# Kernel tuning notes

Hardware: AMD Instinct MI355X
Metric: run time of the kernel (lower is better)

## Reference

```python
import jax, jax.numpy as jnp
import numpy as np
from jax import lax

B, T, H, W, E = 64, 8, 8, 8, 512
REC = 2048


def setup_inputs() -> dict:
    key = jax.random.key(0)
    kx, kwi, kwr = jax.random.split(key, 3)
    x = jax.random.normal(kx, (B, T, H, W, E), dtype=jnp.float32)
    W_input = jax.random.normal(kwi, (E, REC), dtype=jnp.float32) / np.sqrt(E)
    W_recurrent = jax.random.normal(kwr, (REC, REC), dtype=jnp.float32) / np.sqrt(REC)
    return {"x": x, "W_input": W_input, "W_recurrent": W_recurrent}


def reference(x, W_input, W_recurrent):
    b, t, h, w, e = x.shape
    R = t * h * w
    rec = W_recurrent.shape[0]
    k = int(rec * 0.4)  # 819, matches torch: int(recurrent_size * 0.4)
    x_seq = jnp.swapaxes(x.reshape(b, R, e), 0, 1)  # [R, B, E]
    row_idx = jnp.arange(b)[:, None]

    def step(r, inp):
        z = r @ W_recurrent                    # [B, REC]
        vals, idx = lax.top_k(z, k)            # [B, k]
        s = jnp.zeros_like(z).at[row_idx, idx].set(vals)  # scatter top-k back
        r_new = jnp.tanh(inp @ W_input + s)
        r_new = r_new / (jnp.linalg.norm(r_new, axis=-1, keepdims=True) + 1e-6)
        return r_new, None

    r0 = jnp.zeros((b, rec), dtype=x.dtype)
    r_final, _ = lax.scan(step, r0, x_seq)
    return r_final
```

## Files before the change

### kernel.cpp

```cpp
#include <hip/hip_runtime.h>

#define NSTEP 512
#define EDIM  512
#define REC   2048
#define NB    64
#define KSEL  819
#define KC    8
#define ZCH   256
#define AP    264
#define CSTR  16896

typedef unsigned short u16;
typedef __bf16 bf16x8 __attribute__((ext_vector_type(8)));
typedef float  f32x4  __attribute__((ext_vector_type(4)));
typedef unsigned long long ull;

static __device__ __forceinline__ f32x4 mfma16(bf16x8 a, bf16x8 b, f32x4 c) {
    return __builtin_amdgcn_mfma_f32_16x16x32_bf16(a, b, c, 0, 0, 0);
}

static __device__ __forceinline__ void split2(float v, u16& c0, u16& c1) {
    __bf16 b0 = (__bf16)v;
    __bf16 b1 = (__bf16)(v - (float)b0);
    c0 = __builtin_bit_cast(u16, b0);
    c1 = __builtin_bit_cast(u16, b1);
}

static __device__ __forceinline__ void cstore4f(float* p, float v) {
    __hip_atomic_store((unsigned*)p, __float_as_uint(v), __ATOMIC_RELAXED, __HIP_MEMORY_SCOPE_AGENT);
}
static __device__ __forceinline__ void cstore4u(unsigned* p, unsigned v) {
    __hip_atomic_store(p, v, __ATOMIC_RELAXED, __HIP_MEMORY_SCOPE_AGENT);
}
static __device__ __forceinline__ unsigned cload4u(const unsigned* p) {
    return __hip_atomic_load(p, __ATOMIC_RELAXED, __HIP_MEMORY_SCOPE_AGENT);
}
static __device__ __forceinline__ void cstore8u(void* p, ull v) {
    __hip_atomic_store((ull*)p, v, __ATOMIC_RELAXED, __HIP_MEMORY_SCOPE_AGENT);
}
static __device__ __forceinline__ ull cload8u(const void* p) {
    return __hip_atomic_load((const ull*)p, __ATOMIC_RELAXED, __HIP_MEMORY_SCOPE_AGENT);
}
static __device__ __forceinline__ float2 cload8f(const float* p) {
    ull u = cload8u(p);
    float2 v; __builtin_memcpy(&v, &u, 8);
    return v;
}

__device__ __forceinline__ void gbar(unsigned* bar, int bid, unsigned gen)
{
    __syncthreads();
    if (threadIdx.x == 0) {
        const int g = bid >> 4, idx = bid & 15;
        cstore4u(&bar[g * 32 + idx], gen);
        if (idx == 0) {
            const ull* slots = (const ull*)&bar[g * 32];
            for (;;) {
                bool ok = true;
#pragma unroll
                for (int i = 0; i < 8; ++i) {
                    const ull v = cload8u(&slots[i]);
                    if ((unsigned)v < gen || (unsigned)(v >> 32) < gen) ok = false;
                }
                if (ok) break;
                __builtin_amdgcn_s_sleep(1);
            }
            cstore4u(&bar[512 + g], gen);
            if (bid == 0) {
                const ull* rs = (const ull*)&bar[512];
                for (;;) {
                    bool ok = true;
#pragma unroll
                    for (int i = 0; i < 8; ++i) {
                        const ull v = cload8u(&rs[i]);
                        if ((unsigned)v < gen || (unsigned)(v >> 32) < gen) ok = false;
                    }
                    if (ok) break;
                    __builtin_amdgcn_s_sleep(1);
                }
#pragma unroll
                for (int gg = 0; gg < 16; ++gg)
                    cstore4u(&bar[1024 + gg * 32], gen);
            }
        }
        while (cload4u(&bar[1024 + g * 32]) < gen)
            __builtin_amdgcn_s_sleep(1);
        __asm__ volatile("" ::: "memory");
    }
    __syncthreads();
}

__global__ __launch_bounds__(512, 1)
void rnn_persistent(const float* __restrict__ x, const float* __restrict__ Wi,
                    const float* __restrict__ Wr, float* __restrict__ out,
                    u16* __restrict__ rTu, float* __restrict__ zb,
                    u16* __restrict__ Ybf, unsigned* __restrict__ bar)
{
    extern __shared__ __align__(16) char smem[];
    u16* WrSu = (u16*)smem;
    u16* aSu  = (u16*)(smem + 67584);
    float* WiP = (float*)smem;
    float* xP  = (float*)(smem + 16384);
    unsigned*      kS    = (unsigned*)(smem + 67584);
    unsigned char* selS  = (unsigned char*)(smem + 67584 + 8192);
    unsigned*      hist  = (unsigned*)(smem + 67584 + 10240);
    __shared__ unsigned s_byte, s_newrem, s_cnteq;
    __shared__ float red[8];
    __shared__ float s_norm;

    const int bid = blockIdx.x;
    const int tid = threadIdx.x;
    const int kc = bid & 7, nc = bid >> 3;
    const int n0 = nc * 64, kcbase = kc * ZCH;
    const int wid = tid >> 6, lane = tid & 63;
    const int q = lane >> 4, l16 = lane & 15;
    const int Moff = (wid & 3) * 16, Npair = wid >> 2;
    unsigned gen = 0;

    {
        const int t0 = bid * 2;
        const int tr4 = (tid >> 5) * 4;
        const int tc4 = (tid & 31) * 4;
        for (int nc2 = 0; nc2 < 16; ++nc2) {
            const int n0y = nc2 * 128;
            f32x4 acc[2][4];
#pragma unroll
            for (int h = 0; h < 2; ++h)
#pragma unroll
                for (int i = 0; i < 4; ++i) acc[h][i] = (f32x4){0,0,0,0};
            for (int kr = 0; kr < 16; ++kr) {
                const int k0y = kr * 32;
                __syncthreads();
                {
                    const int col4 = (tid & 31) * 4, row = tid >> 5;
                    *(float4*)&WiP[row * 128 + col4] =
                        *(const float4*)(Wi + (long long)(k0y + row) * REC + n0y + col4);
                    *(float4*)&WiP[(row + 16) * 128 + col4] =
                        *(const float4*)(Wi + (long long)(k0y + row + 16) * REC + n0y + col4);
                }
                for (int h = 0; h < 2; ++h) {
                    __syncthreads();
                    {
                        const int b = tid & 63, e4 = (tid >> 6) * 4;
                        const float4 v = *(const float4*)(x + ((long long)b * NSTEP + (t0 + h)) * EDIM + k0y + e4);
                        xP[(e4    ) * 64 + b] = v.x;
                        xP[(e4 + 1) * 64 + b] = v.y;
                        xP[(e4 + 2) * 64 + b] = v.z;
                        xP[(e4 + 3) * 64 + b] = v.w;
                    }
                    __syncthreads();
#pragma unroll 8
                    for (int kk = 0; kk < 32; ++kk) {
                        const float4 af = *(const float4*)&xP[kk * 64 + tr4];
                        const float4 bf = *(const float4*)&WiP[kk * 128 + tc4];
                        const float av[4] = {af.x, af.y, af.z, af.w};
#pragma unroll
                        for (int i = 0; i < 4; ++i) {
                            acc[h][i].x += av[i] * bf.x;
                            acc[h][i].y += av[i] * bf.y;
                            acc[h][i].z += av[i] * bf.z;
                            acc[h][i].w += av[i] * bf.w;
                        }
                    }
                }
            }
#pragma unroll
            for (int h = 0; h < 2; ++h)
#pragma unroll
                for (int i = 0; i < 4; ++i) {
                    const long long yrow = (long long)(t0 + h) * 64 + tr4 + i;
                    u16 o[4];
                    o[0] = __builtin_bit_cast(u16, (__bf16)acc[h][i].x);
                    o[1] = __builtin_bit_cast(u16, (__bf16)acc[h][i].y);
                    o[2] = __builtin_bit_cast(u16, (__bf16)acc[h][i].z);
                    o[3] = __builtin_bit_cast(u16, (__bf16)acc[h][i].w);
                    ull pk; __builtin_memcpy(&pk, o, 8);
                    cstore8u(&Ybf[yrow * REC + n0y + tc4], pk);
                }
        }
    }
    {
        const int g = bid * 512 + tid;
        if (g < 65536) cstore8u(rTu + (long long)g * 4, 0ull);
        cstore4f(zb + g, 0.f);
    }
    ++gen; gbar(bar, bid, gen);

    {
        for (int it = 0; it < 32; ++it) {
            const int row = it * 8 + wid;
            const int col = lane;
            const float v = Wr[(long long)(kcbase + row) * REC + n0 + col];
            u16 s0, s1; split2(v, s0, s1);
            const int base = col * AP + row;
            WrSu[base] = s0;
            WrSu[CSTR + base] = s1;
        }
        __syncthreads();
    }

    const int hw = tid >> 5, hl = tid & 31;
    for (int t = 0; t < NSTEP; ++t) {
        float* zcur = zb + (size_t)(t & 1) * 131072;
        float* znxt = zb + (size_t)((t + 1) & 1) * 131072;
        cstore4f(znxt + bid * 512 + tid, 0.f);
        {
            ull va[8], vbv[8];
#pragma unroll
            for (int i = 0; i < 8; ++i) {
                const int c = i >> 2;
                const int b = (i & 3) * 16 + hw;
                const u16* src = rTu + (long long)c * 131072 + (long long)b * REC + kcbase + hl * 8;
                va[i] = cload8u(src);
                vbv[i] = cload8u(src + 4);
            }
#pragma unroll
            for (int i = 0; i < 8; ++i) {
                const int c = i >> 2;
                const int b = (i & 3) * 16 + hw;
                u16* dst = aSu + c * CSTR + b * AP + hl * 8;
                *(ull*)dst = va[i];
                *(ull*)(dst + 4) = vbv[i];
            }
        }
        __syncthreads();

        f32x4 acc0 = {0,0,0,0}, acc1 = {0,0,0,0};
#pragma unroll
        for (int ks = 0; ks < 8; ++ks) {
            const int kk = ks * 32 + q * 8;
            const u16* ap = aSu + (Moff + l16) * AP + kk;
            bf16x8 A0 = *(const bf16x8*)(ap);
            bf16x8 A1 = *(const bf16x8*)(ap + CSTR);
            const u16* bp0 = WrSu + (Npair * 32 + l16) * AP + kk;
            bf16x8 B00 = *(const bf16x8*)(bp0);
            bf16x8 B01 = *(const bf16x8*)(bp0 + CSTR);
            const u16* bp1 = bp0 + 16 * AP;
            bf16x8 B10 = *(const bf16x8*)(bp1);
            bf16x8 B11 = *(const bf16x8*)(bp1 + CSTR);
            acc0 = mfma16(A0, B00, acc0);
            acc1 = mfma16(A0, B10, acc1);
            acc0 = mfma16(A0, B01, acc0);
            acc1 = mfma16(A0, B11, acc1);
            acc0 = mfma16(A1, B00, acc0);
            acc1 = mfma16(A1, B10, acc1);
        }
        {
            const int colA = n0 + Npair * 32 + l16;
#pragma unroll
            for (int i = 0; i < 4; ++i) {
                float* zp = zcur + (long long)(Moff + q * 4 + i) * REC + colA;
                unsafeAtomicAdd(zp,      ((float*)&acc0)[i]);
                unsafeAtomicAdd(zp + 16, ((float*)&acc1)[i]);
            }
        }
        ++gen; gbar(bar, bid, gen);

        if (bid < NB) {
            const int b = bid;
            const int j0 = tid * 4;
            float zs[4];
            {
                const float2 u0 = cload8f(zcur + (long long)b * REC + j0);
                const float2 u1 = cload8f(zcur + (long long)b * REC + j0 + 2);
                zs[0] = u0.x; zs[1] = u0.y; zs[2] = u1.x; zs[3] = u1.y;
            }
            const ushort4 yv = *(const ushort4*)&Ybf[((long long)t * 64 + b) * REC + j0];
            unsigned kv[4];
#pragma unroll
            for (int s = 0; s < 4; ++s) {
                const unsigned u = __float_as_uint(zs[s]);
                kv[s] = (u & 0x80000000u) ? ~u : (u | 0x80000000u);
            }
            *(uint4*)&kS[j0] = *(uint4*)kv;
            unsigned* hw_ = hist + wid * 256;
            unsigned prefix = 0, remaining = KSEL;
            int done = 0;
            for (int byte = 3; byte >= 0 && !done; --byte) {
                {
                    uint4 zz = {0u, 0u, 0u, 0u};
                    *(uint4*)&hw_[lane * 4] = zz;
                }
                const int shift = byte * 8;
                const unsigned pmask = (byte == 3) ? 0u : (0xFFFFFFFFu << (shift + 8));
#pragma unroll
                for (int s = 0; s < 4; ++s) {
                    if ((kv[s] & pmask) == prefix)
                        atomicAdd(&hw_[(kv[s] >> shift) & 255u], 1u);
                }
                __syncthreads();
                if (tid < 64) {
                    unsigned c0 = 0, c1 = 0, c2 = 0, c3 = 0;
#pragma unroll
                    for (int w = 0; w < 8; ++w) {
                        const uint4 hv = *(const uint4*)&hist[w * 256 + tid * 4];
                        c0 += hv.x; c1 += hv.y; c2 += hv.z; c3 += hv.w;
                    }
                    const unsigned tot = c0 + c1 + c2 + c3;
                    unsigned suf = tot;
#pragma unroll
                    for (int st = 1; st < 64; st <<= 1) {
                        unsigned o = __shfl_down(suf, (unsigned)st);
                        if (tid + st >= 64) o = 0u;
                        suf += o;
                    }
                    unsigned S[5];
                    S[0] = suf; S[1] = suf - c0; S[2] = suf - c0 - c1;
                    S[3] = suf - c0 - c1 - c2; S[4] = suf - tot;
                    const unsigned cc[4] = {c0, c1, c2, c3};
#pragma unroll
                    for (int qq = 0; qq < 4; ++qq) {
                        if (S[qq] >= remaining && S[qq + 1] < remaining) {
                            s_byte = (unsigned)(tid * 4 + qq);
                            s_newrem = remaining - S[qq + 1];
                            s_cnteq = cc[qq];
                        }
                    }
                }
                __syncthreads();
                prefix |= (s_byte << shift);
                remaining = s_newrem;
                if (remaining == s_cnteq) done = 1;
            }
            unsigned char sel[4];
            if (done) {
#pragma unroll
                for (int s = 0; s < 4; ++s)
                    sel[s] = (kv[s] >= prefix) ? 1 : 0;
            } else {
                if (tid == 0) {
                    unsigned rem = remaining;
                    const unsigned T = prefix;
                    for (int j = 0; j < REC; ++j) {
                        const unsigned k = kS[j];
                        unsigned char sl = 0;
                        if (k > T) sl = 1;
                        else if (k == T && rem > 0u) { sl = 1; --rem; }
                        selS[j] = sl;
                    }
                }
                __syncthreads();
#pragma unroll
                for (int s = 0; s < 4; ++s) sel[s] = selS[j0 + s];
            }
            float rn[4]; float ss = 0.f;
            const u16 ya[4] = {yv.x, yv.y, yv.z, yv.w};
#pragma unroll
            for (int s = 0; s < 4; ++s) {
                const float y = __uint_as_float(((unsigned)ya[s]) << 16);
                const float v = y + (sel[s] ? zs[s] : 0.f);
                const float th = tanhf(v);
                rn[s] = th; ss += th * th;
            }
#pragma unroll
            for (int off = 32; off > 0; off >>= 1)
                ss += __shfl_down(ss, (unsigned)off);
            if (lane == 0) red[wid] = ss;
            __syncthreads();
            if (tid == 0) {
                float a = 0.f;
#pragma unroll
                for (int i = 0; i < 8; ++i) a += red[i];
                s_norm = sqrtf(a) + 1e-6f;
            }
            __syncthreads();
            const float inv = 1.0f / s_norm;
            u16 o0[4], o1[4];
#pragma unroll
            for (int s = 0; s < 4; ++s) {
                const float v = rn[s] * inv;
                split2(v, o0[s], o1[s]);
                if (t == NSTEP - 1) out[(long long)b * REC + j0 + s] = v;
            }
            ull p0, p1;
            __builtin_memcpy(&p0, o0, 8); __builtin_memcpy(&p1, o1, 8);
            cstore8u(rTu + (long long)b * REC + j0, p0);
            cstore8u(rTu + 131072 + (long long)b * REC + j0, p1);
        }
        ++gen; gbar(bar, bid, gen);
    }
}

extern "C" void kernel_launch(void* const* d_in, const int* in_sizes, int n_in,
                              void* d_out, int out_size, void* d_ws, size_t ws_size,
                              hipStream_t stream)
{
    const float* x   = (const float*)d_in[0];
    const float* Win = (const float*)d_in[1];
    const float* Wr  = (const float*)d_in[2];
    float* out = (float*)d_out;

    char* ws = (char*)d_ws;
    const size_t BAR = 8192;
    unsigned* bar = (unsigned*)ws;
    float* zb  = (float*)(ws + BAR);
    u16*   rTu = (u16*)(ws + BAR + 2 * 524288);
    u16*   Ybf = (u16*)(ws + BAR + 2 * 524288 + 524288);

    static int smem_set = 0;
    if (!smem_set) {
        hipFuncSetAttribute((const void*)rnn_persistent,
                            hipFuncAttributeMaxDynamicSharedMemorySize, 135168);
        smem_set = 1;
    }
    hipMemsetAsync(bar, 0, BAR, stream);
    rnn_persistent<<<256, 512, 135168, stream>>>(x, Win, Wr, out, rTu, zb, Ybf, bar);
}
```

Baseline: 8.742 ms.

## Split grid barrier into flat arrive barrier and partial selection barrier

Replaces the two-level hierarchical grid barrier with a flat barrier where one wavefront of block 0 polls all arrival slots at once. After the matmul phase, only the top-k/normalize blocks wait, and other blocks go straight on. The second barrier only waits on arrivals from those 64 blocks. Also moves the kS shared store into the rare fallback path, drops one __syncthreads in the norm reduction, and writes the output as float4. This cuts per-step barrier latency, at the cost of a more delicate generation/ordering scheme.

```diff
diff --git a/kernel.cpp b/kernel.cpp
--- a/kernel.cpp
+++ b/kernel.cpp
@@ -47,43 +47,49 @@
     return v;
 }
 
-__device__ __forceinline__ void gbar(unsigned* bar, int bid, unsigned gen)
+__device__ __forceinline__ void gbarA(unsigned* bar, int bid, int tid,
+                                      unsigned gen, bool wait)
 {
     __syncthreads();
-    if (threadIdx.x == 0) {
-        const int g = bid >> 4, idx = bid & 15;
-        cstore4u(&bar[g * 32 + idx], gen);
-        if (idx == 0) {
-            const ull* slots = (const ull*)&bar[g * 32];
-            for (;;) {
-                bool ok = true;
-#pragma unroll
-                for (int i = 0; i < 8; ++i) {
-                    const ull v = cload8u(&slots[i]);
-                    if ((unsigned)v < gen || (unsigned)(v >> 32) < gen) ok = false;
-                }
-                if (ok) break;
+    if (tid == 0) cstore4u(&bar[bid], gen);
+    if (bid == 0 && tid < 64) {
+        const ull* sl = (const ull*)bar;
+        for (;;) {
+            const ull v0 = cload8u(&sl[tid * 2]);
+            const ull v1 = cload8u(&sl[tid * 2 + 1]);
+            const bool ok = ((unsigned)v0 >= gen) && ((unsigned)(v0 >> 32) >= gen)
+                         && ((unsigned)v1 >= gen) && ((unsigned)(v1 >> 32) >= gen);
+            if (__all(ok)) break;
+            __builtin_amdgcn_s_sleep(1);
+        }
+        if (tid < 16) cstore4u(&bar[1024 + tid * 32], gen);
+    }
+    if (wait) {
+        if (tid == 0) {
+            const int g = bid >> 4;
+            while (cload4u(&bar[1024 + g * 32]) < gen)
                 __builtin_amdgcn_s_sleep(1);
-            }
-            cstore4u(&bar[512 + g], gen);
-            if (bid == 0) {
-                const ull* rs = (const ull*)&bar[512];
-                for (;;) {
-                    bool ok = true;
-#pragma unroll
-                    for (int i = 0; i < 8; ++i) {
-                        const ull v = cload8u(&rs[i]);
-                        if ((unsigned)v < gen || (unsigned)(v >> 32) < gen) ok = false;
-                    }
-                    if (ok) break;
-                    __builtin_amdgcn_s_sleep(1);
-                }
-#pragma unroll
-                for (int gg = 0; gg < 16; ++gg)
-                    cstore4u(&bar[1024 + gg * 32], gen);
-            }
-        }
-        while (cload4u(&bar[1024 + g * 32]) < gen)
+            __asm__ volatile("" ::: "memory");
+        }
+        __syncthreads();
+    }
+}
+
+__device__ __forceinline__ void gbarB(unsigned* bar, int bid, int tid, unsigned gen)
+{
+    __syncthreads();
+    if (bid < NB && tid == 0) cstore4u(&bar[512 + bid], gen);
+    if (bid == 0 && tid < 64) {
+        for (;;) {
+            const unsigned v = cload4u(&bar[512 + tid]);
+            if (__all(v >= gen)) break;
+            __builtin_amdgcn_s_sleep(1);
+        }
+        if (tid < 16) cstore4u(&bar[1536 + tid * 32], gen);
+    }
+    if (tid == 0) {
+        const int g = bid >> 4;
+        while (cload4u(&bar[1536 + g * 32]) < gen)
             __builtin_amdgcn_s_sleep(1);
         __asm__ volatile("" ::: "memory");
     }
@@ -106,7 +112,6 @@
     unsigned*      hist  = (unsigned*)(smem + 67584 + 10240);
     __shared__ unsigned s_byte, s_newrem, s_cnteq;
     __shared__ float red[8];
-    __shared__ float s_norm;
 
     const int bid = blockIdx.x;
     const int tid = threadIdx.x;
@@ -115,7 +120,7 @@
     const int wid = tid >> 6, lane = tid & 63;
     const int q = lane >> 4, l16 = lane & 15;
     const int Moff = (wid & 3) * 16, Npair = wid >> 2;
-    unsigned gen = 0;
+    const bool isB = (bid < NB);
 
     {
         const int t0 = bid * 2;
@@ -184,7 +189,7 @@
         if (g < 65536) cstore8u(rTu + (long long)g * 4, 0ull);
         cstore4f(zb + g, 0.f);
     }
-    ++gen; gbar(bar, bid, gen);
+    gbarA(bar, bid, tid, 1u, true);
 
     {
         for (int it = 0; it < 32; ++it) {
@@ -254,9 +259,9 @@
                 unsafeAtomicAdd(zp + 16, ((float*)&acc1)[i]);
             }
         }
-        ++gen; gbar(bar, bid, gen);
-
-        if (bid < NB) {
+        gbarA(bar, bid, tid, (unsigned)(t + 2), isB);
+
+        if (isB) {
             const int b = bid;
             const int j0 = tid * 4;
             float zs[4];
@@ -272,7 +277,6 @@
                 const unsigned u = __float_as_uint(zs[s]);
                 kv[s] = (u & 0x80000000u) ? ~u : (u | 0x80000000u);
             }
-            *(uint4*)&kS[j0] = *(uint4*)kv;
             unsigned* hw_ = hist + wid * 256;
             unsigned prefix = 0, remaining = KSEL;
             int done = 0;
@@ -328,6 +332,8 @@
                 for (int s = 0; s < 4; ++s)
                     sel[s] = (kv[s] >= prefix) ? 1 : 0;
             } else {
+                *(uint4*)&kS[j0] = *(uint4*)kv;
+                __syncthreads();
                 if (tid == 0) {
                     unsigned rem = remaining;
                     const unsigned T = prefix;
@@ -357,27 +363,26 @@
                 ss += __shfl_down(ss, (unsigned)off);
             if (lane == 0) red[wid] = ss;
             __syncthreads();
-            if (tid == 0) {
-                float a = 0.f;
-#pragma unroll
-                for (int i = 0; i < 8; ++i) a += red[i];
-                s_norm = sqrtf(a) + 1e-6f;
-            }
-            __syncthreads();
-            const float inv = 1.0f / s_norm;
+            float a = 0.f;
+#pragma unroll
+            for (int i = 0; i < 8; ++i) a += red[i];
+            const float inv = 1.0f / (sqrtf(a) + 1e-6f);
             u16 o0[4], o1[4];
+            float4 ov;
 #pragma unroll
             for (int s = 0; s < 4; ++s) {
                 const float v = rn[s] * inv;
                 split2(v, o0[s], o1[s]);
-                if (t == NSTEP - 1) out[(long long)b * REC + j0 + s] = v;
+                ((float*)&ov)[s] = v;
             }
             ull p0, p1;
             __builtin_memcpy(&p0, o0, 8); __builtin_memcpy(&p1, o1, 8);
             cstore8u(rTu + (long long)b * REC + j0, p0);
             cstore8u(rTu + 131072 + (long long)b * REC + j0, p1);
-        }
-        ++gen; gbar(bar, bid, gen);
+            if (t == NSTEP - 1)
+                *(float4*)&out[(long long)b * REC + j0] = ov;
+        }
+        gbarB(bar, bid, tid, (unsigned)(t + 1));
     }
 }
 
```

After: 7.687 ms. -12.1%, faster.
